# Kernel tuning notes

Measured on AMD Instinct MI355X. Metric: run time of the kernel, lower is better.

Reference implementation:

```python
import jax, jax.numpy as jnp
import numpy as np

NUM_EMBEDDINGS = 8192
EMBEDDING_DIM = 256
COMMITMENT_COST = 0.25


def setup_inputs() -> dict:
    key = jax.random.key(0)
    k1, k2 = jax.random.split(key)
    x = jax.random.normal(k1, (8, 4096, EMBEDDING_DIM), dtype=jnp.float32)
    # torch init: uniform(-1/K, 1/K)
    codebook = jax.random.uniform(
        k2, (NUM_EMBEDDINGS, EMBEDDING_DIM), dtype=jnp.float32,
        minval=-1.0 / NUM_EMBEDDINGS, maxval=1.0 / NUM_EMBEDDINGS)
    return {"x": x, "codebook": codebook}


def reference(x, codebook):
    D = codebook.shape[1]
    K = codebook.shape[0]
    flat_x = x.reshape(-1, D)                      # [N, D]
    distances = (jnp.sum(flat_x * flat_x, axis=1, keepdims=True)
                 + jnp.sum(codebook * codebook, axis=1)
                 - 2.0 * jnp.matmul(flat_x, codebook.T))
    encoding_indices = jnp.argmin(distances, axis=1)  # [N]
    # direct gather instead of one-hot matmul (same math)
    quantized = codebook[encoding_indices].reshape(x.shape)

    sg = jax.lax.stop_gradient
    e_latent_loss = jnp.mean((sg(quantized) - x) ** 2)
    q_latent_loss = jnp.mean((quantized - sg(x)) ** 2)
    loss = q_latent_loss + COMMITMENT_COST * e_latent_loss

    quantized_st = x + sg(quantized - x)

    # avg one-hot probs via counts
    counts = jnp.bincount(encoding_indices, length=K)
    avg_probs = counts.astype(x.dtype) / encoding_indices.shape[0]
    perplexity = jnp.exp(-jnp.sum(avg_probs * jnp.log(avg_probs + 1e-10)))
    return quantized_st, loss, perplexity
```

## Files before the change

kernel.cpp:

```cpp
#include <hip/hip_runtime.h>
#include <cfloat>
#include <math.h>

#define NUM_EMB 8192
#define DIM 256
#define NROWS 32768
#define NSPLIT 4
#define CHUNKS 32

typedef float f32x4 __attribute__((ext_vector_type(4)));
typedef int   i32x4 __attribute__((ext_vector_type(4)));
typedef int   i32x8 __attribute__((ext_vector_type(8)));

#define GL2LDS(g, l) __builtin_amdgcn_global_load_lds( \
    (const __attribute__((address_space(1))) void*)(g), \
    (__attribute__((address_space(3))) void*)(l), 16, 0, 0)

#define MFMA(A, B, C) __builtin_amdgcn_mfma_scale_f32_16x16x128_f8f6f4( \
    (A), (B), (C), 0, 0, 0, 127, 0, 127)

#define DSR(dst, addr, IMM) \
    asm volatile("ds_read_b128 %0, %1 offset:%2" : "=v"(dst) : "v"(addr), "n"(IMM))

__global__ __launch_bounds__(256) void vq_prep(const float* __restrict__ x,
                                               unsigned char* __restrict__ xq,
                                               const float* __restrict__ cb,
                                               unsigned char* __restrict__ cbq,
                                               float* __restrict__ cbn,
                                               unsigned int* __restrict__ counts) {
    int b = blockIdx.x;
    if (b < 2048) {
        #pragma unroll
        for (int j = 0; j < 2; j++) {
            int i = b * 512 + j * 256 + threadIdx.x;
            float4 v0 = ((const float4*)x)[2 * i];
            float4 v1 = ((const float4*)x)[2 * i + 1];
            int p0 = __builtin_amdgcn_cvt_pk_fp8_f32(-v0.x, -v0.y, 0, false);
            p0     = __builtin_amdgcn_cvt_pk_fp8_f32(-v0.z, -v0.w, p0, true);
            int p1 = __builtin_amdgcn_cvt_pk_fp8_f32(-v1.x, -v1.y, 0, false);
            p1     = __builtin_amdgcn_cvt_pk_fp8_f32(-v1.z, -v1.w, p1, true);
            ((int2*)xq)[i] = make_int2(p0, p1);
        }
    } else if (b < 4096) {
        int row  = (b - 2048) * 4 + (threadIdx.x >> 6);
        int lane = threadIdx.x & 63;
        float4 v = ((const float4*)(cb + (size_t)row * DIM))[lane];
        int p = __builtin_amdgcn_cvt_pk_fp8_f32(v.x * 8192.f, v.y * 8192.f, 0, false);
        p     = __builtin_amdgcn_cvt_pk_fp8_f32(v.z * 8192.f, v.w * 8192.f, p, true);
        ((int*)cbq)[row * 64 + lane] = p;
        float s = v.x * v.x + v.y * v.y + v.z * v.z + v.w * v.w;
        #pragma unroll
        for (int off = 32; off > 0; off >>= 1) s += __shfl_down(s, off, 64);
        if (lane == 0) cbn[row] = 4096.f * s + 256.f;
    } else {
        counts[(b - 4096) * 256 + threadIdx.x] = 0u;
    }
}

__global__ __launch_bounds__(256, 4) void vq_argmin_mfma(
        const unsigned char* __restrict__ xq,
        const unsigned char* __restrict__ cbq,
        const float* __restrict__ cbn,
        unsigned long long* __restrict__ partial) {
    __shared__ __align__(16) unsigned char Bs[2][16384];
    __shared__ unsigned long long redk[2][64];

    const int tid = threadIdx.x;
    const int lane = tid & 63;
    const int w = tid >> 6;
    const int wm = w >> 1, wn = w & 1;
    const int l15 = lane & 15, q = lane >> 4;
    const int ns = blockIdx.x & (NSPLIT - 1);
    const int by = blockIdx.x >> 2;
    const int m0 = by * 64;
    const int nbase = ns * (NUM_EMB / NSPLIT);

    i32x8 afr00, afr01, afr10, afr11;
    {
        const unsigned char* p = xq + (size_t)(m0 + wm * 32 + l15) * 256 + q * 32;
        i32x4 lo, hi;
        lo = *(const i32x4*)(p);                  hi = *(const i32x4*)(p + 16);
        afr00 = __builtin_shufflevector(lo, hi, 0, 1, 2, 3, 4, 5, 6, 7);
        lo = *(const i32x4*)(p + 16 * 256);       hi = *(const i32x4*)(p + 16 * 256 + 16);
        afr01 = __builtin_shufflevector(lo, hi, 0, 1, 2, 3, 4, 5, 6, 7);
        lo = *(const i32x4*)(p + 128);            hi = *(const i32x4*)(p + 128 + 16);
        afr10 = __builtin_shufflevector(lo, hi, 0, 1, 2, 3, 4, 5, 6, 7);
        lo = *(const i32x4*)(p + 16 * 256 + 128); hi = *(const i32x4*)(p + 16 * 256 + 128 + 16);
        afr11 = __builtin_shufflevector(lo, hi, 0, 1, 2, 3, 4, 5, 6, 7);
    }

    const int row0 = wn * 32 + l15;
    const int sw = row0 & 7;
    const int vA = row0 * 256 + (((2 * q) ^ sw) * 16);
    const int vB = row0 * 256 + (((2 * q + 1) ^ sw) * 16);
    const unsigned lbase =
        (unsigned)(size_t)(__attribute__((address_space(3))) void*)(void*)&Bs[0][0];
    const int addrA = (int)(lbase + (unsigned)vA);
    const int addrB = (int)(lbase + (unsigned)vB);

    const unsigned int colb0 = (unsigned)(wn * 32 + l15);
    const unsigned int colb1 = colb0 + 16;

    unsigned int runk[2][4];
    #pragma unroll
    for (int i = 0; i < 2; i++)
        #pragma unroll
        for (int r = 0; r < 4; r++) runk[i][r] = 0xFFFFFFFFu;

    const int sr = lane >> 4;
    const int sv = lane & 15;
    const int kcs = sv >> 3, blk = sv & 7;
    const unsigned char* gs[4];
    int sg[4];
    #pragma unroll
    for (int t = 0; t < 4; t++) {
        int s = t * 4 + w;
        int r = s * 4 + sr;
        gs[t] = cbq + (size_t)(nbase + r) * 256 + (size_t)(kcs * 128 + ((blk ^ (r & 7)) * 16));
        sg[t] = s * 1024;
    }

    #pragma unroll
    for (int t = 0; t < 4; t++) GL2LDS(gs[t], (char*)&Bs[0][0] + sg[t]);
    #pragma unroll
    for (int t = 0; t < 4; t++) gs[t] += 16384;
    const float* bnp = cbn + nbase;
    float bn0 = bnp[colb0];
    float bn1 = bnp[colb1];
    __syncthreads();

#define CHUNK_BODY(CHV, CUR, NXT, LAST) do { \
    float nbn0 = bnp[64 + (int)colb0]; \
    float nbn1 = bnp[64 + (int)colb1]; \
    if (!(LAST)) { \
        GL2LDS(gs[0], (char*)&Bs[NXT][0] + sg[0]); \
        GL2LDS(gs[1], (char*)&Bs[NXT][0] + sg[1]); \
        GL2LDS(gs[2], (char*)&Bs[NXT][0] + sg[2]); \
        GL2LDS(gs[3], (char*)&Bs[NXT][0] + sg[3]); \
        __builtin_amdgcn_sched_barrier(0); \
    } \
    gs[0] += 16384; gs[1] += 16384; gs[2] += 16384; gs[3] += 16384; \
    f32x4 ci0; ci0[0] = bn0; ci0[1] = bn0; ci0[2] = bn0; ci0[3] = bn0; \
    f32x4 ci1; ci1[0] = bn1; ci1[1] = bn1; ci1[2] = bn1; ci1[3] = bn1; \
    i32x4 b0l, b0h, b1l, b1h, b2l, b2h, b3l, b3h; \
    DSR(b0l, addrA, (CUR) * 16384 + 0); \
    DSR(b0h, addrB, (CUR) * 16384 + 0); \
    DSR(b2l, addrA, (CUR) * 16384 + 4096); \
    DSR(b2h, addrB, (CUR) * 16384 + 4096); \
    DSR(b1l, addrA, (CUR) * 16384 + 128); \
    DSR(b1h, addrB, (CUR) * 16384 + 128); \
    DSR(b3l, addrA, (CUR) * 16384 + 4224); \
    DSR(b3h, addrB, (CUR) * 16384 + 4224); \
    asm volatile("s_waitcnt lgkmcnt(4)" ::: "memory"); \
    __builtin_amdgcn_sched_barrier(0); \
    i32x8 b0 = __builtin_shufflevector(b0l, b0h, 0, 1, 2, 3, 4, 5, 6, 7); \
    i32x8 b2 = __builtin_shufflevector(b2l, b2h, 0, 1, 2, 3, 4, 5, 6, 7); \
    f32x4 a00 = MFMA(afr00, b0, ci0); \
    f32x4 a10 = MFMA(afr01, b0, ci0); \
    f32x4 a01 = MFMA(afr00, b2, ci1); \
    f32x4 a11 = MFMA(afr01, b2, ci1); \
    asm volatile("s_waitcnt lgkmcnt(0)" ::: "memory"); \
    __builtin_amdgcn_sched_barrier(0); \
    i32x8 b1 = __builtin_shufflevector(b1l, b1h, 0, 1, 2, 3, 4, 5, 6, 7); \
    i32x8 b3 = __builtin_shufflevector(b3l, b3h, 0, 1, 2, 3, 4, 5, 6, 7); \
    a00 = MFMA(afr10, b1, a00); \
    a10 = MFMA(afr11, b1, a10); \
    a01 = MFMA(afr10, b3, a01); \
    a11 = MFMA(afr11, b3, a11); \
    unsigned int chb = ((unsigned)(CHV)) << 6; \
    unsigned int cj0 = chb | colb0, cj1 = chb | colb1; \
    _Pragma("unroll") \
    for (int r = 0; r < 4; r++) { \
        unsigned int k00 = (__float_as_uint(a00[r]) & 0xFFFFF800u) | cj0; \
        unsigned int k01 = (__float_as_uint(a01[r]) & 0xFFFFF800u) | cj1; \
        runk[0][r] = min(min(k00, k01), runk[0][r]); \
        unsigned int k10 = (__float_as_uint(a10[r]) & 0xFFFFF800u) | cj0; \
        unsigned int k11 = (__float_as_uint(a11[r]) & 0xFFFFF800u) | cj1; \
        runk[1][r] = min(min(k10, k11), runk[1][r]); \
    } \
    bn0 = nbn0; bn1 = nbn1; bnp += 64; \
    __syncthreads(); \
} while (0)

    #pragma unroll 1
    for (int ch = 0; ch < CHUNKS; ch += 2) {
        CHUNK_BODY(ch,     0, 1, false);
        CHUNK_BODY(ch + 1, 1, 0, (ch + 1) == CHUNKS - 1);
    }

    #pragma unroll
    for (int i = 0; i < 2; i++) {
        #pragma unroll
        for (int r = 0; r < 4; r++) {
            unsigned int rk = runk[i][r];
            unsigned int gcol = (unsigned)nbase + (rk & 0x7FFu);
            unsigned long long key =
                ((unsigned long long)(rk & 0xFFFFF800u) << 32) | gcol;
            #pragma unroll
            for (int off = 8; off >= 1; off >>= 1) {
                unsigned long long o = __shfl_xor(key, off, 16);
                if (o < key) key = o;
            }
            if (l15 == 0) redk[wn][wm * 32 + i * 16 + q * 4 + r] = key;
        }
    }
    __syncthreads();
    if (tid < 64) {
        unsigned long long k0 = redk[0][tid], k1 = redk[1][tid];
        partial[(size_t)ns * NROWS + m0 + tid] = k0 < k1 ? k0 : k1;
    }
}

__global__ __launch_bounds__(256) void vq_out(const float* __restrict__ x,
                                              const float* __restrict__ cb,
                                              const unsigned long long* __restrict__ partial,
                                              float* __restrict__ out,
                                              unsigned int* __restrict__ counts,
                                              double* __restrict__ loss_part) {
    __shared__ float wred[4];
    int wv   = threadIdx.x >> 6;
    int lane = threadIdx.x & 63;
    float wsum = 0.f;
    #pragma unroll
    for (int rr = 0; rr < 4; rr++) {
        int row = blockIdx.x * 16 + wv * 4 + rr;
        unsigned long long k = 0xFFFFFFFFFFFFFFFFull;
        #pragma unroll
        for (int t = 0; t < NSPLIT; t++) {
            unsigned long long v = partial[(size_t)t * NROWS + row];
            if (v < k) k = v;
        }
        int id = (int)(unsigned int)(k & 0xffffffffu);
        float4 qv = ((const float4*)(cb + (size_t)id * DIM))[lane];
        float4 xv = ((const float4*)(x + (size_t)row * DIM))[lane];
        float dx = qv.x - xv.x, dy = qv.y - xv.y, dz = qv.z - xv.z, dw = qv.w - xv.w;
        float4 o;
        o.x = xv.x + dx; o.y = xv.y + dy; o.z = xv.z + dz; o.w = xv.w + dw;
        ((float4*)(out + (size_t)row * DIM))[lane] = o;
        float s = dx * dx + dy * dy + dz * dz + dw * dw;
        #pragma unroll
        for (int o2 = 32; o2 > 0; o2 >>= 1) s += __shfl_down(s, o2, 64);
        if (lane == 0) {
            wsum += s;
            atomicAdd(&counts[id], 1u);
        }
    }
    if (lane == 0) wred[wv] = wsum;
    __syncthreads();
    if (threadIdx.x == 0) {
        loss_part[blockIdx.x] =
            (double)wred[0] + (double)wred[1] + (double)wred[2] + (double)wred[3];
    }
}

__global__ __launch_bounds__(256) void vq_fin(const unsigned int* __restrict__ counts,
                                              const double* __restrict__ loss_part,
                                              float* __restrict__ out_tail) {
    __shared__ double sh[256];
    __shared__ double sl[256];
    int tid = threadIdx.x;
    double h = 0.0;
    for (int k = tid; k < NUM_EMB; k += 256) {
        float p = (float)counts[k] * (1.0f / 32768.0f);
        h += (double)(p * __logf(p + 1e-10f));
    }
    double ls = 0.0;
    for (int b = tid; b < NROWS / 16; b += 256) ls += loss_part[b];
    sh[tid] = h;
    sl[tid] = ls;
    __syncthreads();
    for (int o = 128; o > 0; o >>= 1) {
        if (tid < o) { sh[tid] += sh[tid + o]; sl[tid] += sl[tid + o]; }
        __syncthreads();
    }
    if (tid == 0) {
        double mean = sl[0] / (double)((size_t)NROWS * DIM);
        out_tail[0] = (float)(1.25 * mean);
        out_tail[1] = (float)exp(-sh[0]);
    }
}

extern "C" void kernel_launch(void* const* d_in, const int* in_sizes, int n_in,
                              void* d_out, int out_size, void* d_ws, size_t ws_size,
                              hipStream_t stream) {
    const float* x  = (const float*)d_in[0];
    const float* cb = (const float*)d_in[1];
    char* ws = (char*)d_ws;
    unsigned int* counts   = (unsigned int*)(ws + 256);
    float* cbn             = (float*)(ws + 33024);
    unsigned char* xq      = (unsigned char*)(ws + 65792);
    unsigned char* cbq     = (unsigned char*)(ws + 65792 + 8388608);
    unsigned long long* pp = (unsigned long long*)(ws + 65792 + 8388608 + 2097152);
    double* loss_part      = (double*)(ws + 65792 + 8388608 + 2097152 + 16777216);
    float* out = (float*)d_out;

    vq_prep       <<<4128, 256, 0, stream>>>(x, xq, cb, cbq, cbn, counts);
    vq_argmin_mfma<<<512 * NSPLIT, 256, 0, stream>>>(xq, cbq, cbn, pp);
    vq_out        <<<2048, 256, 0, stream>>>(x, cb, pp, out, counts, loss_part);
    vq_fin        <<<1, 256, 0, stream>>>(counts, loss_part, out + (size_t)NROWS * DIM);
}
```

Baseline: 187.7 us.

## Double M-tile per block to reuse codebook LDS tiles across more rows

Each argmin block now covers 128 query rows instead of 64. Each wave holds four A fragments and issues twice as many MFMAs per codebook chunk loaded into LDS, and the grid is halved. This cuts codebook global-to-LDS traffic and barrier overhead per unit of compute. In exchange it raises register pressure (more accumulators and A fragments) and leaves fewer blocks to spread across CUs.

Result: slower. 426.0 us (+127.0%).

```diff
diff --git a/kernel.cpp b/kernel.cpp
--- a/kernel.cpp
+++ b/kernel.cpp
@@ -63,7 +63,7 @@
         const float* __restrict__ cbn,
         unsigned long long* __restrict__ partial) {
     __shared__ __align__(16) unsigned char Bs[2][16384];
-    __shared__ unsigned long long redk[2][64];
+    __shared__ unsigned long long redk[2][128];
 
     const int tid = threadIdx.x;
     const int lane = tid & 63;
@@ -72,21 +72,18 @@
     const int l15 = lane & 15, q = lane >> 4;
     const int ns = blockIdx.x & (NSPLIT - 1);
     const int by = blockIdx.x >> 2;
-    const int m0 = by * 64;
+    const int m0 = by * 128;
     const int nbase = ns * (NUM_EMB / NSPLIT);
 
-    i32x8 afr00, afr01, afr10, afr11;
-    {
-        const unsigned char* p = xq + (size_t)(m0 + wm * 32 + l15) * 256 + q * 32;
+    i32x8 afr0[4], afr1[4];
+    #pragma unroll
+    for (int i = 0; i < 4; i++) {
+        const unsigned char* p = xq + (size_t)(m0 + wm * 64 + i * 16 + l15) * 256 + q * 32;
         i32x4 lo, hi;
-        lo = *(const i32x4*)(p);                  hi = *(const i32x4*)(p + 16);
-        afr00 = __builtin_shufflevector(lo, hi, 0, 1, 2, 3, 4, 5, 6, 7);
-        lo = *(const i32x4*)(p + 16 * 256);       hi = *(const i32x4*)(p + 16 * 256 + 16);
-        afr01 = __builtin_shufflevector(lo, hi, 0, 1, 2, 3, 4, 5, 6, 7);
-        lo = *(const i32x4*)(p + 128);            hi = *(const i32x4*)(p + 128 + 16);
-        afr10 = __builtin_shufflevector(lo, hi, 0, 1, 2, 3, 4, 5, 6, 7);
-        lo = *(const i32x4*)(p + 16 * 256 + 128); hi = *(const i32x4*)(p + 16 * 256 + 128 + 16);
-        afr11 = __builtin_shufflevector(lo, hi, 0, 1, 2, 3, 4, 5, 6, 7);
+        lo = *(const i32x4*)(p);        hi = *(const i32x4*)(p + 16);
+        afr0[i] = __builtin_shufflevector(lo, hi, 0, 1, 2, 3, 4, 5, 6, 7);
+        lo = *(const i32x4*)(p + 128);  hi = *(const i32x4*)(p + 144);
+        afr1[i] = __builtin_shufflevector(lo, hi, 0, 1, 2, 3, 4, 5, 6, 7);
     }
 
     const int row0 = wn * 32 + l15;
@@ -101,9 +98,9 @@
     const unsigned int colb0 = (unsigned)(wn * 32 + l15);
     const unsigned int colb1 = colb0 + 16;
 
-    unsigned int runk[2][4];
-    #pragma unroll
-    for (int i = 0; i < 2; i++)
+    unsigned int runk[4][4];
+    #pragma unroll
+    for (int i = 0; i < 4; i++)
         #pragma unroll
         for (int r = 0; r < 4; r++) runk[i][r] = 0xFFFFFFFFu;
 
@@ -155,28 +152,31 @@
     __builtin_amdgcn_sched_barrier(0); \
     i32x8 b0 = __builtin_shufflevector(b0l, b0h, 0, 1, 2, 3, 4, 5, 6, 7); \
     i32x8 b2 = __builtin_shufflevector(b2l, b2h, 0, 1, 2, 3, 4, 5, 6, 7); \
-    f32x4 a00 = MFMA(afr00, b0, ci0); \
-    f32x4 a10 = MFMA(afr01, b0, ci0); \
-    f32x4 a01 = MFMA(afr00, b2, ci1); \
-    f32x4 a11 = MFMA(afr01, b2, ci1); \
+    f32x4 acc0[4], acc1[4]; \
+    _Pragma("unroll") \
+    for (int i = 0; i < 4; i++) { \
+        acc0[i] = MFMA(afr0[i], b0, ci0); \
+        acc1[i] = MFMA(afr0[i], b2, ci1); \
+    } \
     asm volatile("s_waitcnt lgkmcnt(0)" ::: "memory"); \
     __builtin_amdgcn_sched_barrier(0); \
     i32x8 b1 = __builtin_shufflevector(b1l, b1h, 0, 1, 2, 3, 4, 5, 6, 7); \
     i32x8 b3 = __builtin_shufflevector(b3l, b3h, 0, 1, 2, 3, 4, 5, 6, 7); \
-    a00 = MFMA(afr10, b1, a00); \
-    a10 = MFMA(afr11, b1, a10); \
-    a01 = MFMA(afr10, b3, a01); \
-    a11 = MFMA(afr11, b3, a11); \
+    _Pragma("unroll") \
+    for (int i = 0; i < 4; i++) { \
+        acc0[i] = MFMA(afr1[i], b1, acc0[i]); \
+        acc1[i] = MFMA(afr1[i], b3, acc1[i]); \
+    } \
     unsigned int chb = ((unsigned)(CHV)) << 6; \
     unsigned int cj0 = chb | colb0, cj1 = chb | colb1; \
     _Pragma("unroll") \
-    for (int r = 0; r < 4; r++) { \
-        unsigned int k00 = (__float_as_uint(a00[r]) & 0xFFFFF800u) | cj0; \
-        unsigned int k01 = (__float_as_uint(a01[r]) & 0xFFFFF800u) | cj1; \
-        runk[0][r] = min(min(k00, k01), runk[0][r]); \
-        unsigned int k10 = (__float_as_uint(a10[r]) & 0xFFFFF800u) | cj0; \
-        unsigned int k11 = (__float_as_uint(a11[r]) & 0xFFFFF800u) | cj1; \
-        runk[1][r] = min(min(k10, k11), runk[1][r]); \
+    for (int i = 0; i < 4; i++) { \
+        _Pragma("unroll") \
+        for (int r = 0; r < 4; r++) { \
+            unsigned int k0 = (__float_as_uint(acc0[i][r]) & 0xFFFFF800u) | cj0; \
+            unsigned int k1 = (__float_as_uint(acc1[i][r]) & 0xFFFFF800u) | cj1; \
+            runk[i][r] = min(min(k0, k1), runk[i][r]); \
+        } \
     } \
     bn0 = nbn0; bn1 = nbn1; bnp += 64; \
     __syncthreads(); \
@@ -189,7 +189,7 @@
     }
 
     #pragma unroll
-    for (int i = 0; i < 2; i++) {
+    for (int i = 0; i < 4; i++) {
         #pragma unroll
         for (int r = 0; r < 4; r++) {
             unsigned int rk = runk[i][r];
@@ -201,11 +201,11 @@
                 unsigned long long o = __shfl_xor(key, off, 16);
                 if (o < key) key = o;
             }
-            if (l15 == 0) redk[wn][wm * 32 + i * 16 + q * 4 + r] = key;
+            if (l15 == 0) redk[wn][wm * 64 + i * 16 + q * 4 + r] = key;
         }
     }
     __syncthreads();
-    if (tid < 64) {
+    if (tid < 128) {
         unsigned long long k0 = redk[0][tid], k1 = redk[1][tid];
         partial[(size_t)ns * NROWS + m0 + tid] = k0 < k1 ? k0 : k1;
     }
@@ -295,7 +295,7 @@
     float* out = (float*)d_out;
 
     vq_prep       <<<4128, 256, 0, stream>>>(x, xq, cb, cbq, cbn, counts);
-    vq_argmin_mfma<<<512 * NSPLIT, 256, 0, stream>>>(xq, cbq, cbn, pp);
+    vq_argmin_mfma<<<256 * NSPLIT, 256, 0, stream>>>(xq, cbq, cbn, pp);
     vq_out        <<<2048, 256, 0, stream>>>(x, cb, pp, out, counts, loss_part);
     vq_fin        <<<1, 256, 0, stream>>>(counts, loss_part, out + (size_t)NROWS * DIM);
 }
```

## Stage codebook norms through LDS and use explicit vmcnt waits with raw barriers

Applied to the files above, without the earlier changes.

The per-chunk codebook norm values now arrive through async global-to-LDS loads alongside the codebook tiles, and are read back with a single ds_read2_b32 instead of per-thread global loads. The implicit __syncthreads (which waits on all outstanding memory) is replaced by explicit s_waitcnt vmcnt(5) plus raw s_barrier. The current chunk's data can then be consumed while the next chunk's prefetch stays in flight. The catch is that correctness now rests on hand-counted vmcnt values and barrier placement, including the wave-wide 4-byte LDS load being complete before other waves read it.

New measurement: 190.8 us. Within noise of the previous version (+1.7%).

```diff
diff --git a/kernel.cpp b/kernel.cpp
--- a/kernel.cpp
+++ b/kernel.cpp
@@ -9,18 +9,25 @@
 #define CHUNKS 32
 
 typedef float f32x4 __attribute__((ext_vector_type(4)));
+typedef float f32x2 __attribute__((ext_vector_type(2)));
 typedef int   i32x4 __attribute__((ext_vector_type(4)));
 typedef int   i32x8 __attribute__((ext_vector_type(8)));
 
 #define GL2LDS(g, l) __builtin_amdgcn_global_load_lds( \
     (const __attribute__((address_space(1))) void*)(g), \
     (__attribute__((address_space(3))) void*)(l), 16, 0, 0)
+#define GL2LDS4(g, l) __builtin_amdgcn_global_load_lds( \
+    (const __attribute__((address_space(1))) void*)(g), \
+    (__attribute__((address_space(3))) void*)(l), 4, 0, 0)
 
 #define MFMA(A, B, C) __builtin_amdgcn_mfma_scale_f32_16x16x128_f8f6f4( \
     (A), (B), (C), 0, 0, 0, 127, 0, 127)
 
 #define DSR(dst, addr, IMM) \
     asm volatile("ds_read_b128 %0, %1 offset:%2" : "=v"(dst) : "v"(addr), "n"(IMM))
+#define DSR2(dst, addr, O0, O1) \
+    asm volatile("ds_read2_b32 %0, %1 offset0:%2 offset1:%3" \
+                 : "=v"(dst) : "v"(addr), "n"(O0), "n"(O1))
 
 __global__ __launch_bounds__(256) void vq_prep(const float* __restrict__ x,
                                                unsigned char* __restrict__ xq,
@@ -63,6 +70,7 @@
         const float* __restrict__ cbn,
         unsigned long long* __restrict__ partial) {
     __shared__ __align__(16) unsigned char Bs[2][16384];
+    __shared__ __align__(16) float bnL[2][64];
     __shared__ unsigned long long redk[2][64];
 
     const int tid = threadIdx.x;
@@ -95,11 +103,14 @@
     const int vB = row0 * 256 + (((2 * q + 1) ^ sw) * 16);
     const unsigned lbase =
         (unsigned)(size_t)(__attribute__((address_space(3))) void*)(void*)&Bs[0][0];
+    const unsigned lbn =
+        (unsigned)(size_t)(__attribute__((address_space(3))) void*)(void*)&bnL[0][0];
     const int addrA = (int)(lbase + (unsigned)vA);
     const int addrB = (int)(lbase + (unsigned)vB);
 
     const unsigned int colb0 = (unsigned)(wn * 32 + l15);
     const unsigned int colb1 = colb0 + 16;
+    const int addrBN = (int)(lbn + 4u * colb0);
 
     unsigned int runk[2][4];
     #pragma unroll
@@ -119,29 +130,32 @@
         gs[t] = cbq + (size_t)(nbase + r) * 256 + (size_t)(kcs * 128 + ((blk ^ (r & 7)) * 16));
         sg[t] = s * 1024;
     }
-
+    const float* bnq = cbn + nbase + lane;
+
+    GL2LDS4(bnq, (char*)&bnL[0][0]);
     #pragma unroll
     for (int t = 0; t < 4; t++) GL2LDS(gs[t], (char*)&Bs[0][0] + sg[t]);
     #pragma unroll
     for (int t = 0; t < 4; t++) gs[t] += 16384;
-    const float* bnp = cbn + nbase;
-    float bn0 = bnp[colb0];
-    float bn1 = bnp[colb1];
-    __syncthreads();
+    bnq += 64;
 
 #define CHUNK_BODY(CHV, CUR, NXT, LAST) do { \
-    float nbn0 = bnp[64 + (int)colb0]; \
-    float nbn1 = bnp[64 + (int)colb1]; \
     if (!(LAST)) { \
+        GL2LDS4(bnq, (char*)&bnL[NXT][0]); \
         GL2LDS(gs[0], (char*)&Bs[NXT][0] + sg[0]); \
         GL2LDS(gs[1], (char*)&Bs[NXT][0] + sg[1]); \
         GL2LDS(gs[2], (char*)&Bs[NXT][0] + sg[2]); \
         GL2LDS(gs[3], (char*)&Bs[NXT][0] + sg[3]); \
-        __builtin_amdgcn_sched_barrier(0); \
+        asm volatile("s_waitcnt vmcnt(5)" ::: "memory"); \
+    } else { \
+        asm volatile("s_waitcnt vmcnt(0)" ::: "memory"); \
     } \
+    __builtin_amdgcn_sched_barrier(0); \
+    __builtin_amdgcn_s_barrier(); \
     gs[0] += 16384; gs[1] += 16384; gs[2] += 16384; gs[3] += 16384; \
-    f32x4 ci0; ci0[0] = bn0; ci0[1] = bn0; ci0[2] = bn0; ci0[3] = bn0; \
-    f32x4 ci1; ci1[0] = bn1; ci1[1] = bn1; ci1[2] = bn1; ci1[3] = bn1; \
+    bnq += 64; \
+    f32x2 bn2; \
+    DSR2(bn2, addrBN, (CUR) * 64, (CUR) * 64 + 16); \
     i32x4 b0l, b0h, b1l, b1h, b2l, b2h, b3l, b3h; \
     DSR(b0l, addrA, (CUR) * 16384 + 0); \
     DSR(b0h, addrB, (CUR) * 16384 + 0); \
@@ -153,6 +167,8 @@
     DSR(b3h, addrB, (CUR) * 16384 + 4224); \
     asm volatile("s_waitcnt lgkmcnt(4)" ::: "memory"); \
     __builtin_amdgcn_sched_barrier(0); \
+    f32x4 ci0; ci0[0] = bn2[0]; ci0[1] = bn2[0]; ci0[2] = bn2[0]; ci0[3] = bn2[0]; \
+    f32x4 ci1; ci1[0] = bn2[1]; ci1[1] = bn2[1]; ci1[2] = bn2[1]; ci1[3] = bn2[1]; \
     i32x8 b0 = __builtin_shufflevector(b0l, b0h, 0, 1, 2, 3, 4, 5, 6, 7); \
     i32x8 b2 = __builtin_shufflevector(b2l, b2h, 0, 1, 2, 3, 4, 5, 6, 7); \
     f32x4 a00 = MFMA(afr00, b0, ci0); \
@@ -178,8 +194,7 @@
         unsigned int k11 = (__float_as_uint(a11[r]) & 0xFFFFF800u) | cj1; \
         runk[1][r] = min(min(k10, k11), runk[1][r]); \
     } \
-    bn0 = nbn0; bn1 = nbn1; bnp += 64; \
-    __syncthreads(); \
+    __builtin_amdgcn_s_barrier(); \
 } while (0)
 
     #pragma unroll 1
```
